# Optimization experiments

Measured on AMD Instinct MI355X. Metric: run time of the kernel, lower is better.

The kernel has to match this reference:

```python
import jax, jax.numpy as jnp
import numpy as np

N_BINS = 64
SIGMA_SCALE = 0.5
_LAB_RANGES = {'L': (0.0, 100.0), 'a': (-128.0, 127.0), 'b': (-128.0, 127.0)}


def _channel_params(vmin, vmax, n_bins=N_BINS, sigma_scale=SIGMA_SCALE):
    delta = (vmax - vmin) / n_bins
    centers = jnp.linspace(vmin + delta / 2, vmax - delta / 2, n_bins, dtype=jnp.float32)
    sigma = jnp.float32(delta * sigma_scale)
    return centers, sigma


def rgb_to_lab(rgb):
    # rgb: (B, 3, H, W) in [0, 1] sRGB
    thr = 0.04045
    lin = jnp.where(rgb > thr, jnp.power((rgb + 0.055) / 1.055, 2.4), rgb / 12.92)
    r, g, b = lin[:, 0], lin[:, 1], lin[:, 2]
    # sRGB -> XYZ (D65)
    x = 0.412453 * r + 0.357580 * g + 0.180423 * b
    y = 0.212671 * r + 0.715160 * g + 0.072169 * b
    z = 0.019334 * r + 0.119193 * g + 0.950227 * b
    xn, zn = 0.950456, 1.088754  # D65 white (Y normalized to 1)
    x = x / xn
    z = z / zn
    eps = 0.008856
    def f(t):
        return jnp.where(t > eps, jnp.cbrt(t), 7.787 * t + 16.0 / 116.0)
    fx, fy, fz = f(x), f(y), f(z)
    L = 116.0 * fy - 16.0
    a = 500.0 * (fx - fy)
    bb = 200.0 * (fy - fz)
    return jnp.stack([L, a, bb], axis=1)  # (B, 3, H, W)


def setup_inputs() -> dict:
    key = jax.random.key(0)
    img = jax.random.uniform(key, (16, 3, 512, 512), dtype=jnp.float32)
    return {"img": img}


def reference(img) -> jnp.ndarray:
    B = img.shape[0]
    img_lab = rgb_to_lab(img)  # (B, 3, H, W)
    parts = []
    for c_idx, name in enumerate(['L', 'a', 'b']):
        centers, sigma = _channel_params(*_LAB_RANGES[name])
        pixels = img_lab[:, c_idx].reshape(B, -1)  # (B, HW)
        diff = pixels[:, :, None] - centers[None, None, :]  # (B, HW, n_bins)
        weights = jnp.exp(-(diff ** 2) / (2.0 * sigma ** 2))
        hist_unnorm = weights.sum(axis=1)  # (B, n_bins)
        hist = hist_unnorm / (hist_unnorm.sum(axis=-1, keepdims=True) + 1e-8)
        parts.append(hist)
    return jnp.concatenate(parts, axis=1)  # (B, 192)
```

## Files before the change

### kernel.cpp

```cpp
#include <hip/hip_runtime.h>
#include <cmath>

#define HW (512*512)
#define NSUB 2048
#define THREADS1 512
#define BLKS_PER_IMG 64

__global__ __launch_bounds__(THREADS1) void count_kernel(const float* __restrict__ img,
                                                         unsigned* __restrict__ cnt) {
    __shared__ unsigned sh[3 * NSUB];
    const int tid = threadIdx.x;
    for (int i = tid; i < 3 * NSUB; i += THREADS1) sh[i] = 0u;
    __syncthreads();

    const int b  = blockIdx.y;
    const int bx = blockIdx.x;
    const float* base = img + (size_t)b * 3u * HW;

    const int stride = BLKS_PER_IMG * THREADS1 * 4;
    for (int p = (bx * THREADS1 + tid) * 4; p < HW; p += stride) {
        float4 r4 = *reinterpret_cast<const float4*>(base + p);
        float4 g4 = *reinterpret_cast<const float4*>(base + p + HW);
        float4 b4 = *reinterpret_cast<const float4*>(base + p + 2 * HW);
        float rr[4] = {r4.x, r4.y, r4.z, r4.w};
        float gg[4] = {g4.x, g4.y, g4.z, g4.w};
        float bl[4] = {b4.x, b4.y, b4.z, b4.w};

        #pragma unroll
        for (int k = 0; k < 4; ++k) {
            float lr = (rr[k] > 0.04045f) ? exp2f(2.4f * log2f((rr[k] + 0.055f) * (1.0f / 1.055f))) : rr[k] * (1.0f / 12.92f);
            float lg = (gg[k] > 0.04045f) ? exp2f(2.4f * log2f((gg[k] + 0.055f) * (1.0f / 1.055f))) : gg[k] * (1.0f / 12.92f);
            float lb = (bl[k] > 0.04045f) ? exp2f(2.4f * log2f((bl[k] + 0.055f) * (1.0f / 1.055f))) : bl[k] * (1.0f / 12.92f);

            float x = 0.4339530f * lr + 0.3762197f * lg + 0.1898288f * lb;
            float y = 0.2126710f * lr + 0.7151600f * lg + 0.0721690f * lb;
            float z = 0.0177578f * lr + 0.1094766f * lg + 0.8727661f * lb;

            float fx = (x > 0.008856f) ? exp2f(log2f(x) * (1.0f/3.0f)) : 7.787f * x + 16.0f/116.0f;
            float fy = (y > 0.008856f) ? exp2f(log2f(y) * (1.0f/3.0f)) : 7.787f * y + 16.0f/116.0f;
            float fz = (z > 0.008856f) ? exp2f(log2f(z) * (1.0f/3.0f)) : 7.787f * z + 16.0f/116.0f;

            int iL = (int)(2375.68f    * fy - 327.68f);
            int iA = (int)(4015.6863f  * (fx - fy) + 1028.01569f);
            int iB = (int)(1606.27451f * (fy - fz) + 1028.01569f);

            atomicAdd(&sh[iL], 1u);
            atomicAdd(&sh[NSUB + iA], 1u);
            atomicAdd(&sh[2 * NSUB + iB], 1u);
        }
    }
    __syncthreads();

    unsigned* dst = cnt + (size_t)b * 3 * NSUB;
    for (int i = tid; i < 3 * NSUB; i += THREADS1) {
        unsigned v = sh[i];
        if (v) atomicAdd(dst + i, v);
    }
}

__global__ __launch_bounds__(256) void conv_norm_kernel(const unsigned* __restrict__ cnt,
                                                        float* __restrict__ out) {
    __shared__ float sub[NSUB];
    __shared__ float hb[64];
    const int img = blockIdx.x / 3;
    const int ch  = blockIdx.x % 3;
    const int t   = threadIdx.x;

    const unsigned* src = cnt + ((size_t)img * 3 + ch) * NSUB;
    for (int i = t; i < NSUB; i += 256) sub[i] = (float)src[i];
    __syncthreads();

    const int j = t >> 2;
    const int q = t & 3;
    const float C = 2.8853901f;
    const float jf = (float)j + 0.5f - (0.5f / 32.0f);
    const int s_lo = 32 * j - 86;
    float acc = 0.0f;
    for (int i = 0; i < 51; ++i) {
        int ii = i + j; if (ii >= 51) ii -= 51;
        int s  = s_lo + q + 4 * ii;
        if ((unsigned)s < (unsigned)NSUB) {
            float d = (float)s * (1.0f / 32.0f) - jf;
            acc += sub[s] * exp2f(-C * d * d);
        }
    }
    acc += __shfl_xor(acc, 1, 64);
    acc += __shfl_xor(acc, 2, 64);
    if (q == 0) hb[j] = acc;
    __syncthreads();

    if (t < 64) {
        float v = hb[t];
        float s = v;
        #pragma unroll
        for (int off = 32; off >= 1; off >>= 1) s += __shfl_down(s, off, 64);
        s = __shfl(s, 0, 64);
        out[img * 192 + ch * 64 + t] = v / (s + 1e-8f);
    }
}

extern "C" void kernel_launch(void* const* d_in, const int* in_sizes, int n_in,
                              void* d_out, int out_size, void* d_ws, size_t ws_size,
                              hipStream_t stream) {
    const float* img = (const float*)d_in[0];
    float* out    = (float*)d_out;
    unsigned* cnt = (unsigned*)d_ws;

    const int B = in_sizes[0] / (3 * HW);

    (void)hipMemsetAsync(cnt, 0, (size_t)B * 3 * NSUB * sizeof(unsigned), stream);
    count_kernel<<<dim3(BLKS_PER_IMG, B), THREADS1, 0, stream>>>(img, cnt);
    conv_norm_kernel<<<B * 3, 256, 0, stream>>>(cnt, out);
}
```

Measured before the change: 100.5 us.

## Replicate shared histograms per wave and replace global atomics with per-block partials

Result: faster. 96.97 us, median of 2 (-3.5%).

```diff
diff --git a/kernel.cpp b/kernel.cpp
--- a/kernel.cpp
+++ b/kernel.cpp
@@ -3,15 +3,18 @@
 
 #define HW (512*512)
 #define NSUB 2048
-#define THREADS1 512
-#define BLKS_PER_IMG 64
+#define THREADS1 1024
+#define BLKS_PER_IMG 32
 
 __global__ __launch_bounds__(THREADS1) void count_kernel(const float* __restrict__ img,
-                                                         unsigned* __restrict__ cnt) {
-    __shared__ unsigned sh[3 * NSUB];
+                                                         unsigned* __restrict__ part) {
+    __shared__ unsigned sh[2][3 * NSUB];
     const int tid = threadIdx.x;
-    for (int i = tid; i < 3 * NSUB; i += THREADS1) sh[i] = 0u;
+    unsigned* flat = &sh[0][0];
+    for (int i = tid; i < 2 * 3 * NSUB; i += THREADS1) flat[i] = 0u;
     __syncthreads();
+
+    unsigned* h = sh[(tid >> 6) & 1];
 
     const int b  = blockIdx.y;
     const int bx = blockIdx.x;
@@ -44,21 +47,18 @@
             int iA = (int)(4015.6863f  * (fx - fy) + 1028.01569f);
             int iB = (int)(1606.27451f * (fy - fz) + 1028.01569f);
 
-            atomicAdd(&sh[iL], 1u);
-            atomicAdd(&sh[NSUB + iA], 1u);
-            atomicAdd(&sh[2 * NSUB + iB], 1u);
+            atomicAdd(&h[iL], 1u);
+            atomicAdd(&h[NSUB + iA], 1u);
+            atomicAdd(&h[2 * NSUB + iB], 1u);
         }
     }
     __syncthreads();
 
-    unsigned* dst = cnt + (size_t)b * 3 * NSUB;
-    for (int i = tid; i < 3 * NSUB; i += THREADS1) {
-        unsigned v = sh[i];
-        if (v) atomicAdd(dst + i, v);
-    }
+    unsigned* dst = part + ((size_t)(b * BLKS_PER_IMG + bx)) * 3 * NSUB;
+    for (int i = tid; i < 3 * NSUB; i += THREADS1) dst[i] = sh[0][i] + sh[1][i];
 }
 
-__global__ __launch_bounds__(256) void conv_norm_kernel(const unsigned* __restrict__ cnt,
+__global__ __launch_bounds__(256) void conv_norm_kernel(const unsigned* __restrict__ part,
                                                         float* __restrict__ out) {
     __shared__ float sub[NSUB];
     __shared__ float hb[64];
@@ -66,8 +66,19 @@
     const int ch  = blockIdx.x % 3;
     const int t   = threadIdx.x;
 
-    const unsigned* src = cnt + ((size_t)img * 3 + ch) * NSUB;
-    for (int i = t; i < NSUB; i += 256) sub[i] = (float)src[i];
+    const unsigned* p0 = part + (size_t)img * BLKS_PER_IMG * 3 * NSUB + (size_t)ch * NSUB;
+    float acc8[8] = {0,0,0,0,0,0,0,0};
+    for (int k = 0; k < BLKS_PER_IMG; ++k) {
+        const unsigned* pk = p0 + (size_t)k * 3 * NSUB + t * 8;
+        uint4 a = *reinterpret_cast<const uint4*>(pk);
+        uint4 c = *reinterpret_cast<const uint4*>(pk + 4);
+        acc8[0] += (float)a.x; acc8[1] += (float)a.y;
+        acc8[2] += (float)a.z; acc8[3] += (float)a.w;
+        acc8[4] += (float)c.x; acc8[5] += (float)c.y;
+        acc8[6] += (float)c.z; acc8[7] += (float)c.w;
+    }
+    #pragma unroll
+    for (int i = 0; i < 8; ++i) sub[t * 8 + i] = acc8[i];
     __syncthreads();
 
     const int j = t >> 2;
@@ -103,12 +114,11 @@
                               void* d_out, int out_size, void* d_ws, size_t ws_size,
                               hipStream_t stream) {
     const float* img = (const float*)d_in[0];
-    float* out    = (float*)d_out;
-    unsigned* cnt = (unsigned*)d_ws;
+    float* out     = (float*)d_out;
+    unsigned* part = (unsigned*)d_ws;
 
     const int B = in_sizes[0] / (3 * HW);
 
-    (void)hipMemsetAsync(cnt, 0, (size_t)B * 3 * NSUB * sizeof(unsigned), stream);
-    count_kernel<<<dim3(BLKS_PER_IMG, B), THREADS1, 0, stream>>>(img, cnt);
-    conv_norm_kernel<<<B * 3, 256, 0, stream>>>(cnt, out);
+    count_kernel<<<dim3(BLKS_PER_IMG, B), THREADS1, 0, stream>>>(img, part);
+    conv_norm_kernel<<<B * 3, 256, 0, stream>>>(part, out);
 }
```
